# Performance work log

Measured on AMD Instinct MI355X. Metric: run time of the kernel, lower is better.

Reference implementation:

```python
import jax, jax.numpy as jnp
import numpy as np

B, N, EMB, H, C = 1, 4096, 256, 4, 64  # heads*C == 256 feeds Linear(256, EMB)
NEG_SLOPE = 0.2
LN_EPS = 1e-5


def setup_inputs() -> dict:
    key = jax.random.key(0)
    ks = jax.random.split(key, 8)
    x = jax.random.normal(ks[0], (B, N, EMB), jnp.float32)
    adj = jax.random.randint(ks[1], (B, N, N), 0, 2, jnp.int32)
    W_lin = jax.random.normal(ks[2], (EMB, H * C), jnp.float32) * (1.0 / EMB) ** 0.5
    att_src = jax.random.normal(ks[3], (H, C), jnp.float32) * 0.1
    att_dst = jax.random.normal(ks[4], (H, C), jnp.float32) * 0.1
    bias_att = jax.random.normal(ks[5], (H * C,), jnp.float32) * 0.02
    W_out = jax.random.normal(ks[6], (H * C, EMB), jnp.float32) * (1.0 / (H * C)) ** 0.5
    b_out = jax.random.normal(ks[7], (EMB,), jnp.float32) * 0.02
    gamma = jnp.ones((EMB,), jnp.float32)
    beta = jnp.zeros((EMB,), jnp.float32)
    return dict(x=x, adj=adj, W_lin=W_lin, att_src=att_src, att_dst=att_dst,
                bias_att=bias_att, W_out=W_out, b_out=b_out, gamma=gamma, beta=beta)


def reference(x, adj, W_lin, att_src, att_dst, bias_att, W_out, b_out, gamma, beta):
    # DenseGATConv (concat=True, add_loop=True, negative_slope=0.2)
    h = (x @ W_lin).reshape(B, N, H, C)                       # [B,N,H,C]
    a_src = jnp.einsum('bnhc,hc->bnh', h, att_src)            # per source node j
    a_dst = jnp.einsum('bnhc,hc->bnh', h, att_dst)            # per dest node i
    # alpha[b,i,j,h] = a_src[b,j,h] + a_dst[b,i,h]
    alpha = a_src[:, None, :, :] + a_dst[:, :, None, :]       # [B,N,N,H]
    alpha = jnp.where(alpha >= 0, alpha, NEG_SLOPE * alpha)   # leaky_relu
    # add self-loops to adjacency, then mask and softmax over source axis j
    idx = jnp.arange(N)
    adj_sl = adj.at[:, idx, idx].set(1)
    alpha = jnp.where(adj_sl[..., None] == 0, -jnp.inf, alpha)
    alpha = jax.nn.softmax(alpha, axis=2)                     # [B,N,N,H]
    out = jnp.einsum('bijh,bjhc->bihc', alpha, h)             # aggregate sources
    out = out.reshape(B, N, H * C) + bias_att                 # concat heads + GAT bias
    # trailing Linear + LayerNorm
    y = out @ W_out + b_out                                   # [B,N,EMB]
    mu = jnp.mean(y, axis=-1, keepdims=True)
    var = jnp.mean((y - mu) ** 2, axis=-1, keepdims=True)
    return (y - mu) * jax.lax.rsqrt(var + LN_EPS) * gamma + beta
```

## Files before the change

kernel.cpp:

```cpp
#include <hip/hip_runtime.h>
#include <stdint.h>

#define N    4096
#define EMB  256
#define NH   4
#define HC   64
#define PAD  40

typedef __attribute__((ext_vector_type(8))) short s16x8;
typedef __attribute__((ext_vector_type(4))) float f32x4;
typedef __attribute__((ext_vector_type(4))) int   i32x4;
typedef unsigned short ushort_t;

__device__ __forceinline__ unsigned short f2bf(float f) {
  unsigned int u = __builtin_bit_cast(unsigned int, f);
  u += 0x7fffu + ((u >> 16) & 1u);
  return (unsigned short)(u >> 16);
}

__global__ void k_transpose_bf(const float* __restrict__ W0, ushort_t* __restrict__ WT0,
                               const float* __restrict__ W1, ushort_t* __restrict__ WT1) {
  int k = blockIdx.x & 255;
  int m = threadIdx.x;
  if (blockIdx.x < 256) WT0[m * EMB + k] = f2bf(W0[k * EMB + m]);
  else                  WT1[m * EMB + k] = f2bf(W1[k * EMB + m]);
}

__global__ __launch_bounds__(256)
void k2_pack(const int* __restrict__ adj, unsigned int* __restrict__ abits) {
  int idx = blockIdx.x * 256 + threadIdx.x;
  int i = idx & (N - 1);
  int jw = idx >> 12;
  const int* src = adj + (size_t)i * N + jw * 32;
  unsigned int word = 0;
  #pragma unroll
  for (int u = 0; u < 8; ++u) {
    i32x4 v = *(const i32x4*)(src + u * 4);
    #pragma unroll
    for (int b = 0; b < 4; ++b)
      word |= (v[b] != 0 ? 1u : 0u) << (u * 4 + b);
  }
  if ((i >> 5) == jw) word |= 1u << (i & 31);
  abits[(size_t)jw * N + i] = word;
}

__global__ __launch_bounds__(256, 2)
void k1_gemm_h(const float* __restrict__ x,
               const ushort_t* __restrict__ WlT,
               const float* __restrict__ att_src,
               const float* __restrict__ att_dst,
               ushort_t* __restrict__ hS,
               float* __restrict__ a_srcT,
               float* __restrict__ a_dstT)
{
  __shared__ ushort_t A_lds[64][PAD];
  __shared__ ushort_t B_lds[64][PAD];
  __shared__ ushort_t T_lds[64][72];
  const int t = threadIdx.x;
  const int lane = t & 63;
  const int w = t >> 6;
  const int i0 = blockIdx.x * 64;
  const int head = blockIdx.y;
  const int c0 = head * 64;
  const int lq = lane >> 4, lm = lane & 15;
  const int srow = t >> 2, sko = (t & 3) * 8;

  f32x4 acc[4];
  #pragma unroll
  for (int nf = 0; nf < 4; ++nf) acc[nf] = f32x4{0.f, 0.f, 0.f, 0.f};

  for (int k0 = 0; k0 < EMB; k0 += 32) {
    __syncthreads();
    {
      const float* src = x + (i0 + srow) * EMB + k0 + sko;
      f32x4 v0 = *(const f32x4*)src;
      f32x4 v1 = *(const f32x4*)(src + 4);
      s16x8 p;
      p[0]=(short)f2bf(v0[0]); p[1]=(short)f2bf(v0[1]); p[2]=(short)f2bf(v0[2]); p[3]=(short)f2bf(v0[3]);
      p[4]=(short)f2bf(v1[0]); p[5]=(short)f2bf(v1[1]); p[6]=(short)f2bf(v1[2]); p[7]=(short)f2bf(v1[3]);
      *(s16x8*)&A_lds[srow][sko] = p;
      *(s16x8*)&B_lds[srow][sko] = *(const s16x8*)(WlT + (c0 + srow) * EMB + k0 + sko);
    }
    __syncthreads();
    s16x8 a = *(const s16x8*)&A_lds[w * 16 + lm][lq * 8];
    #pragma unroll
    for (int nf = 0; nf < 4; ++nf) {
      s16x8 b = *(const s16x8*)&B_lds[nf * 16 + lm][lq * 8];
      acc[nf] = __builtin_amdgcn_mfma_f32_16x16x32_bf16(a, b, acc[nf], 0, 0, 0);
    }
  }

  float ps[4] = {0.f,0.f,0.f,0.f}, pd[4] = {0.f,0.f,0.f,0.f};
  #pragma unroll
  for (int nf = 0; nf < 4; ++nf) {
    float wsv = att_src[c0 + nf * 16 + lm];
    float wdv = att_dst[c0 + nf * 16 + lm];
    #pragma unroll
    for (int r = 0; r < 4; ++r) {
      float v = acc[nf][r];
      int node = w * 16 + lq * 4 + r;
      T_lds[nf * 16 + lm][node] = f2bf(v);
      ps[r] += v * wsv;
      pd[r] += v * wdv;
    }
  }
  #pragma unroll
  for (int r = 0; r < 4; ++r) {
    #pragma unroll
    for (int mm = 1; mm < 16; mm <<= 1) {
      ps[r] += __shfl_xor(ps[r], mm);
      pd[r] += __shfl_xor(pd[r], mm);
    }
  }
  if (lm == 0) {
    #pragma unroll
    for (int r = 0; r < 4; ++r) {
      int node = i0 + w * 16 + lq * 4 + r;
      a_srcT[head * N + node] = ps[r];
      a_dstT[head * N + node] = pd[r];
    }
  }
  __syncthreads();
  {
    int c = t >> 2, seg = t & 3;
    s16x8 v0 = *(const s16x8*)&T_lds[c][seg * 16];
    s16x8 v1 = *(const s16x8*)&T_lds[c][seg * 16 + 8];
    size_t base = (((size_t)head * 128 + (i0 >> 5) + (seg >> 1)) * 64 + c) * 32 + (seg & 1) * 16;
    *(s16x8*)(hS + base) = v0;
    *(s16x8*)(hS + base + 8) = v1;
  }
}

__global__ __launch_bounds__(512, 2)
void k34_attn(const unsigned int* __restrict__ abits,
              const ushort_t* __restrict__ hS,
              const float* __restrict__ a_srcT,
              const float* __restrict__ a_dstT,
              const float* __restrict__ bias_att,
              ushort_t* __restrict__ oat)
{
  __shared__ float acc_lds[2][3][16][65];
  __shared__ float l_lds[2][4][16];

  const int t = threadIdx.x;
  const int lane = t & 63;
  const int w = t >> 6;
  const int hloc = w & 1;
  const int jq = w >> 1;
  const int head = blockIdx.y * 2 + hloc;
  const int i0 = blockIdx.x * 16;
  const int lm = lane & 15, lq = lane >> 4;
  const int ig = i0 + lm;

  const float* asrc_h = a_srcT + head * N;
  const ushort_t* hS_h = hS + (size_t)head * 128 * 64 * 32;
  const float ad = a_dstT[head * N + ig];

  f32x4 acc[4];
  #pragma unroll
  for (int nf = 0; nf < 4; ++nf) acc[nf] = f32x4{0.f, 0.f, 0.f, 0.f};
  float lp = 0.f;

  #pragma unroll 2
  for (int it = 0; it < 32; ++it) {
    const int jw = jq * 32 + it;
    const int jl = jw * 32 + lq * 8;

    unsigned int word = abits[(size_t)jw * N + ig];
    f32x4 as0 = *(const f32x4*)(asrc_h + jl);
    f32x4 as1 = *(const f32x4*)(asrc_h + jl + 4);

    const ushort_t* tile = hS_h + (size_t)jw * 2048;
    s16x8 b0 = *(const s16x8*)(tile + ( 0 + lm) * 32 + lq * 8);
    s16x8 b1 = *(const s16x8*)(tile + (16 + lm) * 32 + lq * 8);
    s16x8 b2 = *(const s16x8*)(tile + (32 + lm) * 32 + lq * 8);
    s16x8 b3 = *(const s16x8*)(tile + (48 + lm) * 32 + lq * 8);

    unsigned int ebits[8];
    #pragma unroll
    for (int jj = 0; jj < 8; ++jj) {
      float asv = (jj < 4) ? as0[jj] : as1[jj - 4];
      float sc = asv + ad;
      sc = fmaxf(sc, 0.2f * sc);
      bool con = (word >> (lq * 8 + jj)) & 1u;
      float e = con ? __expf(sc) : 0.f;
      unsigned int eb = __builtin_bit_cast(unsigned int, e) & 0xffff0000u;
      ebits[jj] = eb;
      lp += __builtin_bit_cast(float, eb);
    }
    i32x4 pk;
    #pragma unroll
    for (int u = 0; u < 4; ++u)
      pk[u] = (int)__builtin_amdgcn_perm(ebits[2 * u + 1], ebits[2 * u], 0x07060302u);
    s16x8 af = __builtin_bit_cast(s16x8, pk);

    acc[0] = __builtin_amdgcn_mfma_f32_16x16x32_bf16(af, b0, acc[0], 0, 0, 0);
    acc[1] = __builtin_amdgcn_mfma_f32_16x16x32_bf16(af, b1, acc[1], 0, 0, 0);
    acc[2] = __builtin_amdgcn_mfma_f32_16x16x32_bf16(af, b2, acc[2], 0, 0, 0);
    acc[3] = __builtin_amdgcn_mfma_f32_16x16x32_bf16(af, b3, acc[3], 0, 0, 0);
  }

  lp += __shfl_xor(lp, 16);
  lp += __shfl_xor(lp, 32);
  if (lq == 0) l_lds[hloc][jq][lm] = lp;

  if (jq != 0) {
    #pragma unroll
    for (int nf = 0; nf < 4; ++nf)
      #pragma unroll
      for (int r = 0; r < 4; ++r)
        acc_lds[hloc][jq - 1][lq * 4 + r][nf * 16 + lm] = acc[nf][r];
  }
  __syncthreads();
  if (jq == 0) {
    float linv[4];
    #pragma unroll
    for (int r = 0; r < 4; ++r) {
      int row = lq * 4 + r;
      linv[r] = 1.f / (l_lds[hloc][0][row] + l_lds[hloc][1][row] +
                       l_lds[hloc][2][row] + l_lds[hloc][3][row]);
    }
    #pragma unroll
    for (int nf = 0; nf < 4; ++nf) {
      float bia = bias_att[head * 64 + nf * 16 + lm];
      #pragma unroll
      for (int r = 0; r < 4; ++r) {
        int row = lq * 4 + r;
        float v = acc[nf][r] + acc_lds[hloc][0][row][nf * 16 + lm]
                             + acc_lds[hloc][1][row][nf * 16 + lm]
                             + acc_lds[hloc][2][row][nf * 16 + lm];
        oat[(size_t)(i0 + row) * EMB + head * 64 + nf * 16 + lm] = f2bf(v * linv[r] + bia);
      }
    }
  }
}

__global__ __launch_bounds__(256, 2)
void k5_gemm_ln(const ushort_t* __restrict__ oat,
                const ushort_t* __restrict__ WoT,
                const float* __restrict__ b_out,
                const float* __restrict__ gamma,
                const float* __restrict__ beta,
                float* __restrict__ out)
{
  __shared__ ushort_t A_lds[16][PAD];
  __shared__ ushort_t B_lds[256][PAD];
  __shared__ float y_lds[16][260];
  const int t = threadIdx.x, lane = t & 63, w = t >> 6;
  const int i0 = blockIdx.x * 16;
  const int lq = lane >> 4, lm = lane & 15;

  f32x4 acc[4];
  #pragma unroll
  for (int nf = 0; nf < 4; ++nf) acc[nf] = f32x4{0.f, 0.f, 0.f, 0.f};

  for (int k0 = 0; k0 < EMB; k0 += 32) {
    __syncthreads();
    if (t < 64) {
      int row = t >> 2, ko = (t & 3) * 8;
      *(s16x8*)&A_lds[row][ko] = *(const s16x8*)(oat + (size_t)(i0 + row) * EMB + k0 + ko);
    }
    {
      const ushort_t* src = WoT + t * EMB + k0;
      #pragma unroll
      for (int u = 0; u < 4; ++u) *(s16x8*)&B_lds[t][u * 8] = *(const s16x8*)(src + u * 8);
    }
    __syncthreads();
    s16x8 a = *(const s16x8*)&A_lds[lm][lq * 8];
    #pragma unroll
    for (int nf = 0; nf < 4; ++nf) {
      s16x8 b = *(const s16x8*)&B_lds[w * 64 + nf * 16 + lm][lq * 8];
      acc[nf] = __builtin_amdgcn_mfma_f32_16x16x32_bf16(a, b, acc[nf], 0, 0, 0);
    }
  }
  #pragma unroll
  for (int nf = 0; nf < 4; ++nf)
    #pragma unroll
    for (int r = 0; r < 4; ++r) {
      int row = lq * 4 + r;
      int col = w * 64 + nf * 16 + lm;
      y_lds[row][col] = acc[nf][r] + b_out[col];
    }
  __syncthreads();
  f32x4 g  = *(const f32x4*)(gamma + lane * 4);
  f32x4 be = *(const f32x4*)(beta + lane * 4);
  #pragma unroll
  for (int r = w * 4; r < w * 4 + 4; ++r) {
    f32x4 v = *(const f32x4*)&y_lds[r][lane * 4];
    float s1 = v[0] + v[1] + v[2] + v[3];
    float s2 = v[0]*v[0] + v[1]*v[1] + v[2]*v[2] + v[3]*v[3];
    #pragma unroll
    for (int mm = 1; mm < 64; mm <<= 1) { s1 += __shfl_xor(s1, mm); s2 += __shfl_xor(s2, mm); }
    float mu = s1 * (1.f / 256.f);
    float var = s2 * (1.f / 256.f) - mu * mu;
    float rs = rsqrtf(var + 1e-5f);
    f32x4 o;
    #pragma unroll
    for (int u = 0; u < 4; ++u) o[u] = (v[u] - mu) * rs * g[u] + be[u];
    *(f32x4*)(out + (size_t)(i0 + r) * EMB + lane * 4) = o;
  }
}

extern "C" void kernel_launch(void* const* d_in, const int* in_sizes, int n_in,
                              void* d_out, int out_size, void* d_ws, size_t ws_size,
                              hipStream_t stream)
{
  (void)in_sizes; (void)n_in; (void)out_size; (void)ws_size;
  const float* x        = (const float*)d_in[0];
  const int*   adj      = (const int*)d_in[1];
  const float* W_lin    = (const float*)d_in[2];
  const float* att_src  = (const float*)d_in[3];
  const float* att_dst  = (const float*)d_in[4];
  const float* bias_att = (const float*)d_in[5];
  const float* W_out    = (const float*)d_in[6];
  const float* b_out    = (const float*)d_in[7];
  const float* gamma    = (const float*)d_in[8];
  const float* beta     = (const float*)d_in[9];
  float* out = (float*)d_out;

  uint8_t* p = (uint8_t*)d_ws;
  ushort_t* WlT = (ushort_t*)p;  p += (size_t)EMB * EMB * sizeof(ushort_t);
  ushort_t* WoT = (ushort_t*)p;  p += (size_t)EMB * EMB * sizeof(ushort_t);
  ushort_t* hS  = (ushort_t*)p;  p += (size_t)NH * HC * N * sizeof(ushort_t);
  float* a_srcb = (float*)p;     p += (size_t)NH * N * sizeof(float);
  float* a_dstb = (float*)p;     p += (size_t)NH * N * sizeof(float);
  ushort_t* oat = (ushort_t*)p;  p += (size_t)N * EMB * sizeof(ushort_t);
  unsigned int* abits = (unsigned int*)p; p += (size_t)(N / 32) * N * sizeof(unsigned int);

  k_transpose_bf<<<2 * EMB, EMB, 0, stream>>>(W_lin, WlT, W_out, WoT);
  k2_pack<<<(N / 32) * N / 256, 256, 0, stream>>>(adj, abits);
  k1_gemm_h<<<dim3(N / 64, NH), 256, 0, stream>>>(x, WlT, att_src, att_dst, hS, a_srcb, a_dstb);
  k34_attn<<<dim3(N / 16, 2), 512, 0, stream>>>(abits, hS, a_srcb, a_dstb, bias_att, oat);
  k5_gemm_ln<<<N / 16, 256, 0, stream>>>(oat, WoT, b_out, gamma, beta, out);
}
```

Before: 181.8 us.

## Repack weights, ballot-pack adjacency, split attention across eight j-waves per head

Weights are stored in a k-blocked packed layout so GEMM B-tile loads become contiguous. The adjacency packer now reads each row coalesced and builds the mask with wave ballots instead of per-thread strided int4 loads. The projection GEMM uses 32-row blocks with a cross-wave reduction of the attention logits. The attention kernel gives each block one head, spreading the source axis over eight waves. It also computes the softmax denominator with an extra MFMA against a ones vector instead of scalar adds. These changes target the memory-bound adjacency pass and raise occupancy, at the cost of larger LDS reductions and one more MFMA per iteration.

```diff
diff --git a/kernel.cpp b/kernel.cpp
--- a/kernel.cpp
+++ b/kernel.cpp
@@ -8,6 +8,7 @@
 #define PAD  40
 
 typedef __attribute__((ext_vector_type(8))) short s16x8;
+typedef __attribute__((ext_vector_type(4))) short s16x4;
 typedef __attribute__((ext_vector_type(4))) float f32x4;
 typedef __attribute__((ext_vector_type(4))) int   i32x4;
 typedef unsigned short ushort_t;
@@ -18,88 +19,88 @@
   return (unsigned short)(u >> 16);
 }
 
-__global__ void k_transpose_bf(const float* __restrict__ W0, ushort_t* __restrict__ WT0,
-                               const float* __restrict__ W1, ushort_t* __restrict__ WT1) {
+__global__ void k_transpose_bf(const float* __restrict__ W0, ushort_t* __restrict__ WP0,
+                               const float* __restrict__ W1, ushort_t* __restrict__ WP1) {
   int k = blockIdx.x & 255;
   int m = threadIdx.x;
-  if (blockIdx.x < 256) WT0[m * EMB + k] = f2bf(W0[k * EMB + m]);
-  else                  WT1[m * EMB + k] = f2bf(W1[k * EMB + m]);
+  unsigned short v;
+  size_t dst = ((size_t)(k >> 5) * 256 + m) * 32 + (k & 31);
+  if (blockIdx.x < 256) { v = f2bf(W0[k * EMB + m]); WP0[dst] = v; }
+  else                  { v = f2bf(W1[k * EMB + m]); WP1[dst] = v; }
 }
 
 __global__ __launch_bounds__(256)
 void k2_pack(const int* __restrict__ adj, unsigned int* __restrict__ abits) {
-  int idx = blockIdx.x * 256 + threadIdx.x;
-  int i = idx & (N - 1);
-  int jw = idx >> 12;
-  const int* src = adj + (size_t)i * N + jw * 32;
-  unsigned int word = 0;
-  #pragma unroll
-  for (int u = 0; u < 8; ++u) {
-    i32x4 v = *(const i32x4*)(src + u * 4);
-    #pragma unroll
-    for (int b = 0; b < 4; ++b)
-      word |= (v[b] != 0 ? 1u : 0u) << (u * 4 + b);
-  }
-  if ((i >> 5) == jw) word |= 1u << (i & 31);
-  abits[(size_t)jw * N + i] = word;
-}
-
-__global__ __launch_bounds__(256, 2)
+  const int w = threadIdx.x >> 6, lane = threadIdx.x & 63;
+  const int i = blockIdx.x * 4 + w;
+  const int* row = adj + (size_t)i * N;
+  #pragma unroll 2
+  for (int c = 0; c < 64; ++c) {
+    int v = row[c * 64 + lane];
+    unsigned long long m = __ballot(v != 0);
+    if ((i >> 6) == c) m |= 1ull << (i & 63);
+    if (lane == 0)      abits[(size_t)(2 * c)     * N + i] = (unsigned int)m;
+    else if (lane == 1) abits[(size_t)(2 * c + 1) * N + i] = (unsigned int)(m >> 32);
+  }
+}
+
+__global__ __launch_bounds__(256, 4)
 void k1_gemm_h(const float* __restrict__ x,
-               const ushort_t* __restrict__ WlT,
+               const ushort_t* __restrict__ WlP,
                const float* __restrict__ att_src,
                const float* __restrict__ att_dst,
                ushort_t* __restrict__ hS,
                float* __restrict__ a_srcT,
                float* __restrict__ a_dstT)
 {
-  __shared__ ushort_t A_lds[64][PAD];
+  __shared__ ushort_t A_lds[32][PAD];
   __shared__ ushort_t B_lds[64][PAD];
-  __shared__ ushort_t T_lds[64][72];
+  __shared__ ushort_t T_lds[64][PAD];
+  __shared__ float red_lds[2][2][32];
   const int t = threadIdx.x;
   const int lane = t & 63;
   const int w = t >> 6;
-  const int i0 = blockIdx.x * 64;
+  const int ihalf = w & 1, chalf = w >> 1;
+  const int i0 = blockIdx.x * 32;
   const int head = blockIdx.y;
   const int c0 = head * 64;
   const int lq = lane >> 4, lm = lane & 15;
-  const int srow = t >> 2, sko = (t & 3) * 8;
-
-  f32x4 acc[4];
-  #pragma unroll
-  for (int nf = 0; nf < 4; ++nf) acc[nf] = f32x4{0.f, 0.f, 0.f, 0.f};
-
-  for (int k0 = 0; k0 < EMB; k0 += 32) {
+
+  f32x4 acc[2];
+  acc[0] = f32x4{0.f, 0.f, 0.f, 0.f};
+  acc[1] = f32x4{0.f, 0.f, 0.f, 0.f};
+
+  for (int kp = 0; kp < 8; ++kp) {
     __syncthreads();
     {
-      const float* src = x + (i0 + srow) * EMB + k0 + sko;
-      f32x4 v0 = *(const f32x4*)src;
-      f32x4 v1 = *(const f32x4*)(src + 4);
-      s16x8 p;
-      p[0]=(short)f2bf(v0[0]); p[1]=(short)f2bf(v0[1]); p[2]=(short)f2bf(v0[2]); p[3]=(short)f2bf(v0[3]);
-      p[4]=(short)f2bf(v1[0]); p[5]=(short)f2bf(v1[1]); p[6]=(short)f2bf(v1[2]); p[7]=(short)f2bf(v1[3]);
-      *(s16x8*)&A_lds[srow][sko] = p;
-      *(s16x8*)&B_lds[srow][sko] = *(const s16x8*)(WlT + (c0 + srow) * EMB + k0 + sko);
+      int row = t >> 3, ko = (t & 7) * 4;
+      f32x4 v = *(const f32x4*)(x + (size_t)(i0 + row) * EMB + kp * 32 + ko);
+      s16x4 pk;
+      pk[0] = (short)f2bf(v[0]); pk[1] = (short)f2bf(v[1]);
+      pk[2] = (short)f2bf(v[2]); pk[3] = (short)f2bf(v[3]);
+      *(s16x4*)&A_lds[row][ko] = pk;
+      *(s16x8*)&B_lds[t >> 2][(t & 3) * 8] =
+          *(const s16x8*)(WlP + (size_t)kp * 8192 + (size_t)c0 * 32 + t * 8);
     }
     __syncthreads();
-    s16x8 a = *(const s16x8*)&A_lds[w * 16 + lm][lq * 8];
-    #pragma unroll
-    for (int nf = 0; nf < 4; ++nf) {
-      s16x8 b = *(const s16x8*)&B_lds[nf * 16 + lm][lq * 8];
+    s16x8 a = *(const s16x8*)&A_lds[ihalf * 16 + lm][lq * 8];
+    #pragma unroll
+    for (int nf = 0; nf < 2; ++nf) {
+      s16x8 b = *(const s16x8*)&B_lds[chalf * 32 + nf * 16 + lm][lq * 8];
       acc[nf] = __builtin_amdgcn_mfma_f32_16x16x32_bf16(a, b, acc[nf], 0, 0, 0);
     }
   }
 
   float ps[4] = {0.f,0.f,0.f,0.f}, pd[4] = {0.f,0.f,0.f,0.f};
   #pragma unroll
-  for (int nf = 0; nf < 4; ++nf) {
-    float wsv = att_src[c0 + nf * 16 + lm];
-    float wdv = att_dst[c0 + nf * 16 + lm];
+  for (int nf = 0; nf < 2; ++nf) {
+    int c = chalf * 32 + nf * 16 + lm;
+    float wsv = att_src[c0 + c];
+    float wdv = att_dst[c0 + c];
     #pragma unroll
     for (int r = 0; r < 4; ++r) {
       float v = acc[nf][r];
-      int node = w * 16 + lq * 4 + r;
-      T_lds[nf * 16 + lm][node] = f2bf(v);
+      T_lds[c][ihalf * 16 + lq * 4 + r] = f2bf(v);
       ps[r] += v * wsv;
       pd[r] += v * wdv;
     }
@@ -115,23 +116,25 @@
   if (lm == 0) {
     #pragma unroll
     for (int r = 0; r < 4; ++r) {
-      int node = i0 + w * 16 + lq * 4 + r;
-      a_srcT[head * N + node] = ps[r];
-      a_dstT[head * N + node] = pd[r];
+      int node = ihalf * 16 + lq * 4 + r;
+      red_lds[0][chalf][node] = ps[r];
+      red_lds[1][chalf][node] = pd[r];
     }
   }
   __syncthreads();
+  if (t < 32) {
+    a_srcT[head * N + i0 + t] = red_lds[0][0][t] + red_lds[0][1][t];
+    a_dstT[head * N + i0 + t] = red_lds[1][0][t] + red_lds[1][1][t];
+  }
   {
     int c = t >> 2, seg = t & 3;
-    s16x8 v0 = *(const s16x8*)&T_lds[c][seg * 16];
-    s16x8 v1 = *(const s16x8*)&T_lds[c][seg * 16 + 8];
-    size_t base = (((size_t)head * 128 + (i0 >> 5) + (seg >> 1)) * 64 + c) * 32 + (seg & 1) * 16;
-    *(s16x8*)(hS + base) = v0;
-    *(s16x8*)(hS + base + 8) = v1;
-  }
-}
-
-__global__ __launch_bounds__(512, 2)
+    s16x8 v = *(const s16x8*)&T_lds[c][seg * 8];
+    size_t base = (((size_t)head * 128 + (i0 >> 5)) * 64 + c) * 32 + seg * 8;
+    *(s16x8*)(hS + base) = v;
+  }
+}
+
+__global__ __launch_bounds__(512, 4)
 void k34_attn(const unsigned int* __restrict__ abits,
               const ushort_t* __restrict__ hS,
               const float* __restrict__ a_srcT,
@@ -139,15 +142,13 @@
               const float* __restrict__ bias_att,
               ushort_t* __restrict__ oat)
 {
-  __shared__ float acc_lds[2][3][16][65];
-  __shared__ float l_lds[2][4][16];
+  __shared__ float acc_lds[7][16][65];
+  __shared__ float l_lds[8][16];
 
   const int t = threadIdx.x;
   const int lane = t & 63;
-  const int w = t >> 6;
-  const int hloc = w & 1;
-  const int jq = w >> 1;
-  const int head = blockIdx.y * 2 + hloc;
+  const int jq = t >> 6;
+  const int head = blockIdx.y;
   const int i0 = blockIdx.x * 16;
   const int lm = lane & 15, lq = lane >> 4;
   const int ig = i0 + lm;
@@ -159,11 +160,14 @@
   f32x4 acc[4];
   #pragma unroll
   for (int nf = 0; nf < 4; ++nf) acc[nf] = f32x4{0.f, 0.f, 0.f, 0.f};
-  float lp = 0.f;
+  f32x4 accl = f32x4{0.f, 0.f, 0.f, 0.f};
+  s16x8 ones;
+  #pragma unroll
+  for (int u = 0; u < 8; ++u) ones[u] = (short)0x3F80;
 
   #pragma unroll 2
-  for (int it = 0; it < 32; ++it) {
-    const int jw = jq * 32 + it;
+  for (int it = 0; it < 16; ++it) {
+    const int jw = jq * 16 + it;
     const int jl = jw * 32 + lq * 8;
 
     unsigned int word = abits[(size_t)jw * N + ig];
@@ -184,9 +188,7 @@
       sc = fmaxf(sc, 0.2f * sc);
       bool con = (word >> (lq * 8 + jj)) & 1u;
       float e = con ? __expf(sc) : 0.f;
-      unsigned int eb = __builtin_bit_cast(unsigned int, e) & 0xffff0000u;
-      ebits[jj] = eb;
-      lp += __builtin_bit_cast(float, eb);
+      ebits[jj] = __builtin_bit_cast(unsigned int, e) & 0xffff0000u;
     }
     i32x4 pk;
     #pragma unroll
@@ -198,18 +200,19 @@
     acc[1] = __builtin_amdgcn_mfma_f32_16x16x32_bf16(af, b1, acc[1], 0, 0, 0);
     acc[2] = __builtin_amdgcn_mfma_f32_16x16x32_bf16(af, b2, acc[2], 0, 0, 0);
     acc[3] = __builtin_amdgcn_mfma_f32_16x16x32_bf16(af, b3, acc[3], 0, 0, 0);
-  }
-
-  lp += __shfl_xor(lp, 16);
-  lp += __shfl_xor(lp, 32);
-  if (lq == 0) l_lds[hloc][jq][lm] = lp;
-
+    accl   = __builtin_amdgcn_mfma_f32_16x16x32_bf16(af, ones, accl, 0, 0, 0);
+  }
+
+  if (lm == 0) {
+    #pragma unroll
+    for (int r = 0; r < 4; ++r) l_lds[jq][lq * 4 + r] = accl[r];
+  }
   if (jq != 0) {
     #pragma unroll
     for (int nf = 0; nf < 4; ++nf)
       #pragma unroll
       for (int r = 0; r < 4; ++r)
-        acc_lds[hloc][jq - 1][lq * 4 + r][nf * 16 + lm] = acc[nf][r];
+        acc_lds[jq - 1][lq * 4 + r][nf * 16 + lm] = acc[nf][r];
   }
   __syncthreads();
   if (jq == 0) {
@@ -217,8 +220,10 @@
     #pragma unroll
     for (int r = 0; r < 4; ++r) {
       int row = lq * 4 + r;
-      linv[r] = 1.f / (l_lds[hloc][0][row] + l_lds[hloc][1][row] +
-                       l_lds[hloc][2][row] + l_lds[hloc][3][row]);
+      float s = 0.f;
+      #pragma unroll
+      for (int q = 0; q < 8; ++q) s += l_lds[q][row];
+      linv[r] = 1.f / s;
     }
     #pragma unroll
     for (int nf = 0; nf < 4; ++nf) {
@@ -226,9 +231,9 @@
       #pragma unroll
       for (int r = 0; r < 4; ++r) {
         int row = lq * 4 + r;
-        float v = acc[nf][r] + acc_lds[hloc][0][row][nf * 16 + lm]
-                             + acc_lds[hloc][1][row][nf * 16 + lm]
-                             + acc_lds[hloc][2][row][nf * 16 + lm];
+        float v = acc[nf][r];
+        #pragma unroll
+        for (int q = 0; q < 7; ++q) v += acc_lds[q][row][nf * 16 + lm];
         oat[(size_t)(i0 + row) * EMB + head * 64 + nf * 16 + lm] = f2bf(v * linv[r] + bia);
       }
     }
@@ -237,7 +242,7 @@
 
 __global__ __launch_bounds__(256, 2)
 void k5_gemm_ln(const ushort_t* __restrict__ oat,
-                const ushort_t* __restrict__ WoT,
+                const ushort_t* __restrict__ WoP,
                 const float* __restrict__ b_out,
                 const float* __restrict__ gamma,
                 const float* __restrict__ beta,
@@ -254,17 +259,16 @@
   #pragma unroll
   for (int nf = 0; nf < 4; ++nf) acc[nf] = f32x4{0.f, 0.f, 0.f, 0.f};
 
-  for (int k0 = 0; k0 < EMB; k0 += 32) {
+  for (int kp = 0; kp < 8; ++kp) {
     __syncthreads();
     if (t < 64) {
       int row = t >> 2, ko = (t & 3) * 8;
-      *(s16x8*)&A_lds[row][ko] = *(const s16x8*)(oat + (size_t)(i0 + row) * EMB + k0 + ko);
-    }
-    {
-      const ushort_t* src = WoT + t * EMB + k0;
-      #pragma unroll
-      for (int u = 0; u < 4; ++u) *(s16x8*)&B_lds[t][u * 8] = *(const s16x8*)(src + u * 8);
-    }
+      *(s16x8*)&A_lds[row][ko] = *(const s16x8*)(oat + (size_t)(i0 + row) * EMB + kp * 32 + ko);
+    }
+    #pragma unroll
+    for (int u = 0; u < 4; ++u)
+      *(s16x8*)&B_lds[(t >> 2) + u * 64][(t & 3) * 8] =
+          *(const s16x8*)(WoP + (size_t)kp * 8192 + u * 2048 + t * 8);
     __syncthreads();
     s16x8 a = *(const s16x8*)&A_lds[lm][lq * 8];
     #pragma unroll
@@ -319,17 +323,17 @@
   float* out = (float*)d_out;
 
   uint8_t* p = (uint8_t*)d_ws;
-  ushort_t* WlT = (ushort_t*)p;  p += (size_t)EMB * EMB * sizeof(ushort_t);
-  ushort_t* WoT = (ushort_t*)p;  p += (size_t)EMB * EMB * sizeof(ushort_t);
+  ushort_t* WlP = (ushort_t*)p;  p += (size_t)EMB * EMB * sizeof(ushort_t);
+  ushort_t* WoP = (ushort_t*)p;  p += (size_t)EMB * EMB * sizeof(ushort_t);
   ushort_t* hS  = (ushort_t*)p;  p += (size_t)NH * HC * N * sizeof(ushort_t);
   float* a_srcb = (float*)p;     p += (size_t)NH * N * sizeof(float);
   float* a_dstb = (float*)p;     p += (size_t)NH * N * sizeof(float);
   ushort_t* oat = (ushort_t*)p;  p += (size_t)N * EMB * sizeof(ushort_t);
   unsigned int* abits = (unsigned int*)p; p += (size_t)(N / 32) * N * sizeof(unsigned int);
 
-  k_transpose_bf<<<2 * EMB, EMB, 0, stream>>>(W_lin, WlT, W_out, WoT);
-  k2_pack<<<(N / 32) * N / 256, 256, 0, stream>>>(adj, abits);
-  k1_gemm_h<<<dim3(N / 64, NH), 256, 0, stream>>>(x, WlT, att_src, att_dst, hS, a_srcb, a_dstb);
-  k34_attn<<<dim3(N / 16, 2), 512, 0, stream>>>(abits, hS, a_srcb, a_dstb, bias_att, oat);
-  k5_gemm_ln<<<N / 16, 256, 0, stream>>>(oat, WoT, b_out, gamma, beta, out);
-}
+  k_transpose_bf<<<2 * EMB, EMB, 0, stream>>>(W_lin, WlP, W_out, WoP);
+  k2_pack<<<N / 4, 256, 0, stream>>>(adj, abits);
+  k1_gemm_h<<<dim3(N / 32, NH), 256, 0, stream>>>(x, WlP, att_src, att_dst, hS, a_srcb, a_dstb);
+  k34_attn<<<dim3(N / 16, NH), 512, 0, stream>>>(abits, hS, a_srcb, a_dstb, bias_att, oat);
+  k5_gemm_ln<<<N / 16, 256, 0, stream>>>(oat, WoP, b_out, gamma, beta, out);
+}
```

New measurement: 218.6 us. 1.2x slower.
